# Optimization experiments

Hardware: AMD Instinct MI355X
Metric: run time of the kernel (lower is better)

## Reference

```python
import jax, jax.numpy as jnp
import numpy as np

SMOOTH = 1.0
P = 2
NUM_ITERS = 200  # kornia connected_components num_iterations


def _maxpool3x3(x):
    # F.max_pool2d(x, kernel_size=3, stride=1, padding=1) equivalent (NCHW)
    return jax.lax.reduce_window(
        x, -jnp.inf, jax.lax.max,
        window_dimensions=(1, 1, 3, 3),
        window_strides=(1, 1, 1, 1),
        padding='SAME',
    )


def connected_components(mask_f, num_iterations=NUM_ITERS):
    # kornia-style iterative label propagation on a (B,1,H,W) binary mask.
    # labels initialized to unique pixel ids where mask==1, 0 elsewhere,
    # then 3x3 max-pool propagated, keeping background pinned at 0.
    B, C, H, W = mask_f.shape
    mask = mask_f > 0
    init = jnp.arange(B * C * H * W, dtype=mask_f.dtype).reshape(B, C, H, W)
    out = jnp.where(mask, init, 0.0)

    def body(i, o):
        return jnp.where(mask, _maxpool3x3(o), 0.0)

    return jax.lax.fori_loop(0, num_iterations, body, out)


def setup_inputs() -> dict:
    key = jax.random.key(0)
    k1, k2 = jax.random.split(key)
    B, H, W = 16, 512, 512
    predict = jax.random.uniform(k1, (B, 1, H, W), dtype=jnp.float32)
    target = jax.random.uniform(k2, (B, 1, H, W), dtype=jnp.float32)
    return {"predict": predict, "target": target}


def reference(predict, target):
    B = predict.shape[0]
    # threshold at half of global max -> binary mask (non-differentiable)
    binmask = (predict > (predict.max() / 2)).astype(predict.dtype)
    labels = connected_components(jax.lax.stop_gradient(binmask))

    # torch.numel(torch.unique(labels)) via sort + adjacent-diff count (jit-safe)
    s = jnp.sort(labels.reshape(-1))
    n_unique = 1 + jnp.sum(s[1:] != s[:-1])

    penalty = n_unique.astype(jnp.float32) / B
    penalty = jnp.where(penalty < 1.0, jnp.float32(B), penalty)
    penalty = jnp.minimum(penalty, jnp.float32(B))

    p = predict.reshape(B, -1)
    t = target.reshape(B, -1)
    num = jnp.sum(p * t, axis=1) + SMOOTH
    den = jnp.sum(p ** P + t ** P, axis=1) + SMOOTH
    loss = 1.0 - num / den
    return loss.mean() * penalty  # reduction='mean'
```

## Files before the change

kernel.cpp:

```cpp
#include <hip/hip_runtime.h>
#include <hip/hip_cooperative_groups.h>
#include <stdint.h>

namespace cg = cooperative_groups;

#define NPIX   (16 * 512 * 512)
#define IMG    (512 * 512)
#define NB     16

#define CORE   64
#define HALO   8
#define KIT    8
#define NROUND 25
#define TW     88
#define TH     82
#define TX0    4

#define BM_WORDS  (NPIX / 32)
#define NREP      16
#define SAT       256u
#define MAX3(a, b, c) max(max((a), (b)), (c))

__global__ __launch_bounds__(256) void k_max(const float4* __restrict__ p, unsigned int* umax) {
    unsigned int m = 0;
    int base = blockIdx.x * 1024;
#pragma unroll
    for (int k = 0; k < 4; ++k) {
        float4 v = p[base + k * 256 + threadIdx.x];
        m = max(m, __float_as_uint(v.x));
        m = max(m, __float_as_uint(v.y));
        m = max(m, __float_as_uint(v.z));
        m = max(m, __float_as_uint(v.w));
    }
    for (int o = 32; o > 0; o >>= 1)
        m = max(m, (unsigned int)__shfl_down(m, o, 64));
    __shared__ unsigned int sm[4];
    int lane = threadIdx.x & 63, w = threadIdx.x >> 6;
    if (lane == 0) sm[w] = m;
    __syncthreads();
    if (threadIdx.x == 0)
        atomicMax(umax, max(max(sm[0], sm[1]), max(sm[2], sm[3])));
}

__global__ __launch_bounds__(256) void k_iso(const float* __restrict__ pr,
                                             const unsigned int* __restrict__ umax,
                                             unsigned int* __restrict__ isoCnt) {
    const float thr = __uint_as_float(*umax) * 0.5f;
    unsigned int cnt = 0;
    const int tid = threadIdx.x;
    for (int k = 0; k < 8; ++k) {
        int i4 = (blockIdx.x * 8 + k) * 256 + tid;
        int px = i4 * 4;
        int y   = (px >> 9) & 511;
        int gxr = px & 511;
        float4 c = *(const float4*)(pr + px);
        bool m0 = c.x > thr, m1 = c.y > thr, m2 = c.z > thr, m3 = c.w > thr;
        bool lc = (gxr > 0)   && pr[px - 1] > thr;
        bool rc = (gxr < 508) && pr[px + 4] > thr;
        bool u0 = false, u1 = false, u2 = false, u3 = false, lu = false, ru = false;
        if (y > 0) {
            float4 u = *(const float4*)(pr + px - 512);
            u0 = u.x > thr; u1 = u.y > thr; u2 = u.z > thr; u3 = u.w > thr;
            lu = (gxr > 0)   && pr[px - 513] > thr;
            ru = (gxr < 508) && pr[px - 508] > thr;
        }
        bool d0 = false, d1 = false, d2 = false, d3 = false, ld = false, rd = false;
        if (y < 511) {
            float4 d = *(const float4*)(pr + px + 512);
            d0 = d.x > thr; d1 = d.y > thr; d2 = d.z > thr; d3 = d.w > thr;
            ld = (gxr > 0)   && pr[px + 511] > thr;
            rd = (gxr < 508) && pr[px + 516] > thr;
        }
        bool v0 = u0 | d0, v1 = u1 | d1, v2 = u2 | d2, v3 = u3 | d3;
        bool cmL = lu | lc | ld, cmR = ru | rc | rd;
        bool cm0 = v0 | m0, cm1 = v1 | m1, cm2 = v2 | m2, cm3 = v3 | m3;
        cnt += (m0 && !(cmL | cm1 | v0) && px > 0) ? 1u : 0u;
        cnt += (m1 && !(cm0 | cm2 | v1)) ? 1u : 0u;
        cnt += (m2 && !(cm1 | cm3 | v2)) ? 1u : 0u;
        cnt += (m3 && !(cm2 | cmR | v3)) ? 1u : 0u;
    }
    for (int o = 32; o > 0; o >>= 1)
        cnt += __shfl_down(cnt, o, 64);
    __shared__ unsigned int sc[4];
    int lane = tid & 63, w = tid >> 6;
    if (lane == 0) sc[w] = cnt;
    __syncthreads();
    if (tid == 0)
        atomicAdd(isoCnt, sc[0] + sc[1] + sc[2] + sc[3]);
}

__global__ __launch_bounds__(256) void k_init(const float4* __restrict__ pr4,
                                              const float4* __restrict__ tg4,
                                              const unsigned int* __restrict__ umax,
                                              const unsigned int* __restrict__ isoCnt,
                                              int4* __restrict__ lab4,
                                              float* __restrict__ num, float* __restrict__ den) {
    const float thr = __uint_as_float(*umax) * 0.5f;
    const bool wlab = (*isoCnt < SAT);
    float sn = 0.f, sd = 0.f;
    int base = blockIdx.x * 1024;
#pragma unroll
    for (int k = 0; k < 4; ++k) {
        int i4 = base + k * 256 + threadIdx.x;
        float4 p = pr4[i4], t = tg4[i4];
        if (wlab) {
            int pix = i4 * 4;
            int4 L;
            L.x = (p.x > thr) ? pix     : -1;
            L.y = (p.y > thr) ? pix + 1 : -1;
            L.z = (p.z > thr) ? pix + 2 : -1;
            L.w = (p.w > thr) ? pix + 3 : -1;
            lab4[i4] = L;
        }
        sn += p.x * t.x + p.y * t.y + p.z * t.z + p.w * t.w;
        sd += p.x * p.x + p.y * p.y + p.z * p.z + p.w * p.w
            + t.x * t.x + t.y * t.y + t.z * t.z + t.w * t.w;
    }
    for (int o = 32; o > 0; o >>= 1) {
        sn += __shfl_down(sn, o, 64);
        sd += __shfl_down(sd, o, 64);
    }
    __shared__ float wn[4], wd[4];
    int lane = threadIdx.x & 63, w = threadIdx.x >> 6;
    if (lane == 0) { wn[w] = sn; wd[w] = sd; }
    __syncthreads();
    if (threadIdx.x == 0) {
        int b = blockIdx.x >> 6;
        atomicAdd(&num[b * 32], wn[0] + wn[1] + wn[2] + wn[3]);
        atomicAdd(&den[b * 32], wd[0] + wd[1] + wd[2] + wd[3]);
    }
}

__global__ __launch_bounds__(256, 4) void k_prop_all(int* __restrict__ bufA,
                                                     int* __restrict__ bufB,
                                                     unsigned int* __restrict__ bm,
                                                     const unsigned int* __restrict__ isoCnt) {
    if (*isoCnt >= SAT) return;
    cg::grid_group grid = cg::this_grid();
    __shared__ int T[TH * TW];
    const int tid  = threadIdx.x;
    const int blk  = blockIdx.x;
    const int bx   = blk & 7, by = (blk >> 3) & 7, bimg = blk >> 6;
    const int gx0  = bx * CORE - HALO;
    const int gy0  = by * CORE - HALO;
    int* const base0 = bufA + bimg * IMG;
    int* const base1 = bufB + bimg * IMG;

    {
        int4* bmz = (int4*)bm;
        for (int u = blk * 256 + tid; u < NREP * BM_WORDS / 4; u += 1024 * 256)
            bmz[u] = make_int4(0, 0, 0, 0);
    }

    if (tid < TW) { T[tid] = -1; T[81 * TW + tid] = -1; }
    if (tid < 80) { T[(tid + 1) * TW + 3] = -1; T[(tid + 1) * TW + 84] = -1; }
    for (int u = tid; u < 1600; u += 256) {
        int r = u / 20, c = (u % 20) * 4;
        int gy = gy0 + r, gx = gx0 + c;
        int4 v = (gy >= 0 && gy < 512 && gx >= 0 && gx < 512)
                 ? *(const int4*)(base0 + (gy << 9) + gx)
                 : make_int4(-1, -1, -1, -1);
        *(int4*)&T[(r + 1) * TW + TX0 + c] = v;
    }
    __syncthreads();
    grid.sync();

    const bool active = (tid < 200);
    const int cu = tid % 20, ru = tid / 20;
    const int x0 = cu * 4;
    const int yr = ru * 8;
    int4 O[8];

#define LOAD_ROW(y, V, VL, VR) do {                            \
        const int* _r = &T[((y) + 1) * TW + TX0 + x0];         \
        V  = *(const int4*)_r;                                 \
        VL = _r[-1];                                           \
        VR = _r[4];                                            \
    } while (0)

    for (int r = 0; r < NROUND; ++r) {
        for (int it = 0; it < KIT; ++it) {
            if (active) {
                int4 A, B, C; int Al, Ar, Bl, Br, Cl, Cr;
                LOAD_ROW(yr - 1, A, Al, Ar);
                LOAD_ROW(yr,     B, Bl, Br);
#pragma unroll
                for (int j = 0; j < 8; ++j) {
                    LOAD_ROW(yr + j + 1, C, Cl, Cr);
                    int4 col;
                    col.x = MAX3(A.x, B.x, C.x);
                    col.y = MAX3(A.y, B.y, C.y);
                    col.z = MAX3(A.z, B.z, C.z);
                    col.w = MAX3(A.w, B.w, C.w);
                    int cl = MAX3(Al, Bl, Cl);
                    int cr = MAX3(Ar, Br, Cr);
                    O[j].x = MAX3(cl,    col.x, col.y) | (B.x >> 31);
                    O[j].y = MAX3(col.x, col.y, col.z) | (B.y >> 31);
                    O[j].z = MAX3(col.y, col.z, col.w) | (B.z >> 31);
                    O[j].w = MAX3(col.z, col.w, cr)    | (B.w >> 31);
                    A = B; Al = Bl; Ar = Br;
                    B = C; Bl = Cl; Br = Cr;
                }
            }
            __syncthreads();
            if (active) {
#pragma unroll
                for (int j = 0; j < 8; ++j)
                    *(int4*)&T[(yr + j + 1) * TW + TX0 + x0] = O[j];
            }
            __syncthreads();
        }

        if (r < NROUND - 1) {
            int* dst = (r & 1) ? base1 : base0;
            for (int u = tid; u < 448; u += 256) {
                int lr, lc;
                if (u < 128)      { lr = u >> 4;                lc = u & 15; }
                else if (u < 256) { lr = 56 + ((u - 128) >> 4); lc = u & 15; }
                else { int v = u - 256; lr = 8 + (v >> 2); int s = v & 3; lc = (s < 2) ? s : 12 + s; }
                int4 val = *(const int4*)&T[(HALO + lr + 1) * TW + TX0 + HALO + lc * 4];
                *(int4*)(dst + ((by * CORE + lr) << 9) + bx * CORE + lc * 4) = val;
            }
            __threadfence();
            grid.sync();
            const int* src = (r & 1) ? base1 : base0;
            for (int u = tid; u < 576; u += 256) {
                int lrow, lcu;
                if (u < 160)      { lrow = u / 20;              lcu = u % 20; }
                else if (u < 320) { lrow = 72 + (u - 160) / 20; lcu = u % 20; }
                else { int v = u - 320; lrow = 8 + (v >> 2); int s = v & 3; lcu = (s < 2) ? s : 16 + s; }
                int gy = gy0 + lrow, gx = gx0 + lcu * 4;
                int4 val = (gy >= 0 && gy < 512 && gx >= 0 && gx < 512)
                           ? *(const int4*)(src + (gy << 9) + gx)
                           : make_int4(-1, -1, -1, -1);
                *(int4*)&T[(lrow + 1) * TW + TX0 + lcu * 4] = val;
            }
            __syncthreads();
        } else {
            for (int u = tid; u < 1024; u += 256) {
                int lr = u >> 4, lc = u & 15;
                int4 val = *(const int4*)&T[(HALO + lr + 1) * TW + TX0 + HALO + lc * 4];
                *(int4*)(base0 + ((by * CORE + lr) << 9) + bx * CORE + lc * 4) = val;
            }
        }
    }
#undef LOAD_ROW
}

__global__ __launch_bounds__(256) void k_bits(const int* __restrict__ lab,
                                              unsigned int* __restrict__ bm,
                                              const unsigned int* __restrict__ isoCnt) {
    if (*isoCnt >= SAT) return;
    __shared__ unsigned int sk[1024];
    __shared__ int slot[256];
    const int tid = threadIdx.x;
    unsigned int* rep = bm + (blockIdx.x & (NREP - 1)) * BM_WORDS;
    for (int k = 0; k < 4; ++k) {
        if (k) __syncthreads();
        const int i4 = blockIdx.x * 1024 + k * 256 + tid;
        int4 c = ((const int4*)lab)[i4];
        int pw = __shfl_up(c.w, 1, 64);
        unsigned int prevk;
        if ((tid & 63) == 0) {
            if (i4 == 0) prevk = ~0u;
            else { int pv = lab[i4 * 4 - 1]; prevk = (pv < 0) ? 0u : (unsigned int)pv; }
        } else {
            prevk = (pw < 0) ? 0u : (unsigned int)pw;
        }
        unsigned int k0 = (c.x < 0) ? 0u : (unsigned int)c.x;
        unsigned int k1 = (c.y < 0) ? 0u : (unsigned int)c.y;
        unsigned int k2 = (c.z < 0) ? 0u : (unsigned int)c.z;
        unsigned int k3 = (c.w < 0) ? 0u : (unsigned int)c.w;
        bool c0 = (k0 != prevk), c1 = (k1 != k0), c2 = (k2 != k1), c3 = (k3 != k2);
        sk[0 * 256 + tid] = k0;
        sk[1 * 256 + tid] = k1;
        sk[2 * 256 + tid] = k2;
        sk[3 * 256 + tid] = k3;
        if (c0) slot[k0 & 255] = tid * 4 + 0;
        if (c1) slot[k1 & 255] = tid * 4 + 1;
        if (c2) slot[k2 & 255] = tid * 4 + 2;
        if (c3) slot[k3 & 255] = tid * 4 + 3;
        __syncthreads();
#define SKAT(w) sk[((w) & 3) * 256 + ((w) >> 2)]
        if (c0) { int w = slot[k0 & 255]; if (w != tid * 4 + 0 && SKAT(w) == k0) c0 = false; }
        if (c1) { int w = slot[k1 & 255]; if (w != tid * 4 + 1 && SKAT(w) == k1) c1 = false; }
        if (c2) { int w = slot[k2 & 255]; if (w != tid * 4 + 2 && SKAT(w) == k2) c2 = false; }
        if (c3) { int w = slot[k3 & 255]; if (w != tid * 4 + 3 && SKAT(w) == k3) c3 = false; }
#undef SKAT
#define TSET(kk, cc) if (cc) {                                        \
            unsigned int word = rep[(kk) >> 5];                       \
            if (!((word >> ((kk) & 31)) & 1u))                        \
                atomicOr(&rep[(kk) >> 5], 1u << ((kk) & 31));         \
        }
        TSET(k0, c0); TSET(k1, c1); TSET(k2, c2); TSET(k3, c3);
#undef TSET
    }
}

__global__ void k_popc(const unsigned int* __restrict__ bm, unsigned int* nuniq, int words,
                       const unsigned int* __restrict__ isoCnt) {
    if (*isoCnt >= SAT) return;
    unsigned int c = 0;
    for (int i = blockIdx.x * blockDim.x + threadIdx.x; i < words; i += gridDim.x * blockDim.x) {
        unsigned int w = 0;
#pragma unroll
        for (int r = 0; r < NREP; ++r) w |= bm[r * BM_WORDS + i];
        c += __popc(w);
    }
    for (int o = 32; o > 0; o >>= 1)
        c += __shfl_down(c, o, 64);
    __shared__ unsigned int sc[4];
    int lane = threadIdx.x & 63, w = threadIdx.x >> 6;
    if (lane == 0) sc[w] = c;
    __syncthreads();
    if (threadIdx.x == 0)
        atomicAdd(nuniq, sc[0] + sc[1] + sc[2] + sc[3]);
}

__global__ void k_final(const unsigned int* __restrict__ nuniq,
                        const unsigned int* __restrict__ isoCnt,
                        const float* __restrict__ num, const float* __restrict__ den,
                        float* __restrict__ out) {
    float loss = 0.0f;
    for (int b = 0; b < NB; ++b)
        loss += 1.0f - (num[b * 32] + 1.0f) / (den[b * 32] + 1.0f);
    loss *= (1.0f / NB);
    float penalty;
    if (*isoCnt >= SAT) {
        penalty = (float)NB;
    } else {
        penalty = (float)(*nuniq) / (float)NB;
        if (penalty < 1.0f) penalty = (float)NB;
        penalty = fminf(penalty, (float)NB);
    }
    out[0] = loss * penalty;
}

extern "C" void kernel_launch(void* const* d_in, const int* in_sizes, int n_in,
                              void* d_out, int out_size, void* d_ws, size_t ws_size,
                              hipStream_t stream) {
    const float* predict = (const float*)d_in[0];
    const float* target  = (const float*)d_in[1];
    float* out = (float*)d_out;

    char* ws = (char*)d_ws;
    unsigned int* umax   = (unsigned int*)ws;
    unsigned int* nuniq  = (unsigned int*)(ws + 4);
    unsigned int* isoCnt = (unsigned int*)(ws + 8);
    float* num = (float*)(ws + 256);
    float* den = (float*)(ws + 2304);
    int* labA = (int*)(ws + 16384);
    int* labB = labA + NPIX;
    unsigned int* bm = (unsigned int*)(ws + 16384 + (size_t)2 * NPIX * sizeof(int));

    hipMemsetAsync(ws, 0, 16384, stream);

    k_max<<<1024, 256, 0, stream>>>((const float4*)predict, umax);
    k_iso<<<512, 256, 0, stream>>>(predict, umax, isoCnt);
    k_init<<<1024, 256, 0, stream>>>((const float4*)predict, (const float4*)target,
                                     umax, isoCnt, (int4*)labA, num, den);

    void* args[] = { (void*)&labA, (void*)&labB, (void*)&bm, (void*)&isoCnt };
    hipLaunchCooperativeKernel((void*)k_prop_all, dim3(1024), dim3(256), args, 0, stream);

    k_bits<<<NPIX / 4096, 256, 0, stream>>>(labA, bm, isoCnt);
    k_popc<<<512, 256, 0, stream>>>(bm, nuniq, BM_WORDS, isoCnt);
    k_final<<<1, 1, 0, stream>>>(nuniq, isoCnt, num, den, out);
}
```

Before: 147.2 us.

## Fuse dice sums into max pass and build initial labels inside propagation kernel

```diff
diff --git a/kernel.cpp b/kernel.cpp
--- a/kernel.cpp
+++ b/kernel.cpp
@@ -21,25 +21,42 @@
 #define SAT       256u
 #define MAX3(a, b, c) max(max((a), (b)), (c))
 
-__global__ __launch_bounds__(256) void k_max(const float4* __restrict__ p, unsigned int* umax) {
+__global__ __launch_bounds__(256) void k_maxdice(const float4* __restrict__ pr4,
+                                                 const float4* __restrict__ tg4,
+                                                 unsigned int* __restrict__ umax,
+                                                 float* __restrict__ num,
+                                                 float* __restrict__ den) {
     unsigned int m = 0;
+    float sn = 0.f, sd = 0.f;
     int base = blockIdx.x * 1024;
 #pragma unroll
     for (int k = 0; k < 4; ++k) {
-        float4 v = p[base + k * 256 + threadIdx.x];
-        m = max(m, __float_as_uint(v.x));
-        m = max(m, __float_as_uint(v.y));
-        m = max(m, __float_as_uint(v.z));
-        m = max(m, __float_as_uint(v.w));
-    }
-    for (int o = 32; o > 0; o >>= 1)
-        m = max(m, (unsigned int)__shfl_down(m, o, 64));
+        int i4 = base + k * 256 + threadIdx.x;
+        float4 p = pr4[i4], t = tg4[i4];
+        m = max(m, __float_as_uint(p.x));
+        m = max(m, __float_as_uint(p.y));
+        m = max(m, __float_as_uint(p.z));
+        m = max(m, __float_as_uint(p.w));
+        sn += p.x * t.x + p.y * t.y + p.z * t.z + p.w * t.w;
+        sd += p.x * p.x + p.y * p.y + p.z * p.z + p.w * p.w
+            + t.x * t.x + t.y * t.y + t.z * t.z + t.w * t.w;
+    }
+    for (int o = 32; o > 0; o >>= 1) {
+        m  = max(m, (unsigned int)__shfl_down(m, o, 64));
+        sn += __shfl_down(sn, o, 64);
+        sd += __shfl_down(sd, o, 64);
+    }
     __shared__ unsigned int sm[4];
+    __shared__ float wn[4], wd[4];
     int lane = threadIdx.x & 63, w = threadIdx.x >> 6;
-    if (lane == 0) sm[w] = m;
+    if (lane == 0) { sm[w] = m; wn[w] = sn; wd[w] = sd; }
     __syncthreads();
-    if (threadIdx.x == 0)
+    if (threadIdx.x == 0) {
         atomicMax(umax, max(max(sm[0], sm[1]), max(sm[2], sm[3])));
+        int b = blockIdx.x >> 6;
+        atomicAdd(&num[b * 32], wn[0] + wn[1] + wn[2] + wn[3]);
+        atomicAdd(&den[b * 32], wd[0] + wd[1] + wd[2] + wd[3]);
+    }
 }
 
 __global__ __launch_bounds__(256) void k_iso(const float* __restrict__ pr,
@@ -89,55 +106,16 @@
         atomicAdd(isoCnt, sc[0] + sc[1] + sc[2] + sc[3]);
 }
 
-__global__ __launch_bounds__(256) void k_init(const float4* __restrict__ pr4,
-                                              const float4* __restrict__ tg4,
-                                              const unsigned int* __restrict__ umax,
-                                              const unsigned int* __restrict__ isoCnt,
-                                              int4* __restrict__ lab4,
-                                              float* __restrict__ num, float* __restrict__ den) {
-    const float thr = __uint_as_float(*umax) * 0.5f;
-    const bool wlab = (*isoCnt < SAT);
-    float sn = 0.f, sd = 0.f;
-    int base = blockIdx.x * 1024;
-#pragma unroll
-    for (int k = 0; k < 4; ++k) {
-        int i4 = base + k * 256 + threadIdx.x;
-        float4 p = pr4[i4], t = tg4[i4];
-        if (wlab) {
-            int pix = i4 * 4;
-            int4 L;
-            L.x = (p.x > thr) ? pix     : -1;
-            L.y = (p.y > thr) ? pix + 1 : -1;
-            L.z = (p.z > thr) ? pix + 2 : -1;
-            L.w = (p.w > thr) ? pix + 3 : -1;
-            lab4[i4] = L;
-        }
-        sn += p.x * t.x + p.y * t.y + p.z * t.z + p.w * t.w;
-        sd += p.x * p.x + p.y * p.y + p.z * p.z + p.w * p.w
-            + t.x * t.x + t.y * t.y + t.z * t.z + t.w * t.w;
-    }
-    for (int o = 32; o > 0; o >>= 1) {
-        sn += __shfl_down(sn, o, 64);
-        sd += __shfl_down(sd, o, 64);
-    }
-    __shared__ float wn[4], wd[4];
-    int lane = threadIdx.x & 63, w = threadIdx.x >> 6;
-    if (lane == 0) { wn[w] = sn; wd[w] = sd; }
-    __syncthreads();
-    if (threadIdx.x == 0) {
-        int b = blockIdx.x >> 6;
-        atomicAdd(&num[b * 32], wn[0] + wn[1] + wn[2] + wn[3]);
-        atomicAdd(&den[b * 32], wd[0] + wd[1] + wd[2] + wd[3]);
-    }
-}
-
-__global__ __launch_bounds__(256, 4) void k_prop_all(int* __restrict__ bufA,
+__global__ __launch_bounds__(256, 4) void k_prop_all(const float* __restrict__ pr,
+                                                     int* __restrict__ bufA,
                                                      int* __restrict__ bufB,
                                                      unsigned int* __restrict__ bm,
+                                                     const unsigned int* __restrict__ umax,
                                                      const unsigned int* __restrict__ isoCnt) {
     if (*isoCnt >= SAT) return;
     cg::grid_group grid = cg::this_grid();
     __shared__ int T[TH * TW];
+    const float thr = __uint_as_float(*umax) * 0.5f;
     const int tid  = threadIdx.x;
     const int blk  = blockIdx.x;
     const int bx   = blk & 7, by = (blk >> 3) & 7, bimg = blk >> 6;
@@ -145,6 +123,7 @@
     const int gy0  = by * CORE - HALO;
     int* const base0 = bufA + bimg * IMG;
     int* const base1 = bufB + bimg * IMG;
+    const float* img = pr + bimg * IMG;
 
     {
         int4* bmz = (int4*)bm;
@@ -157,9 +136,15 @@
     for (int u = tid; u < 1600; u += 256) {
         int r = u / 20, c = (u % 20) * 4;
         int gy = gy0 + r, gx = gx0 + c;
-        int4 v = (gy >= 0 && gy < 512 && gx >= 0 && gx < 512)
-                 ? *(const int4*)(base0 + (gy << 9) + gx)
-                 : make_int4(-1, -1, -1, -1);
+        int4 v;
+        if (gy >= 0 && gy < 512 && gx >= 0 && gx < 512) {
+            float4 pv = *(const float4*)(img + (gy << 9) + gx);
+            int id = bimg * IMG + (gy << 9) + gx;
+            v.x = (pv.x > thr) ? id     : -1;
+            v.y = (pv.y > thr) ? id + 1 : -1;
+            v.z = (pv.z > thr) ? id + 2 : -1;
+            v.w = (pv.w > thr) ? id + 3 : -1;
+        } else v = make_int4(-1, -1, -1, -1);
         *(int4*)&T[(r + 1) * TW + TX0 + c] = v;
     }
     __syncthreads();
@@ -353,14 +338,14 @@
     int* labB = labA + NPIX;
     unsigned int* bm = (unsigned int*)(ws + 16384 + (size_t)2 * NPIX * sizeof(int));
 
-    hipMemsetAsync(ws, 0, 16384, stream);
-
-    k_max<<<1024, 256, 0, stream>>>((const float4*)predict, umax);
+    hipMemsetAsync(ws, 0, 8192, stream);
+
+    k_maxdice<<<1024, 256, 0, stream>>>((const float4*)predict, (const float4*)target,
+                                        umax, num, den);
     k_iso<<<512, 256, 0, stream>>>(predict, umax, isoCnt);
-    k_init<<<1024, 256, 0, stream>>>((const float4*)predict, (const float4*)target,
-                                     umax, isoCnt, (int4*)labA, num, den);
-
-    void* args[] = { (void*)&labA, (void*)&labB, (void*)&bm, (void*)&isoCnt };
+
+    void* args[] = { (void*)&predict, (void*)&labA, (void*)&labB,
+                     (void*)&bm, (void*)&umax, (void*)&isoCnt };
     hipLaunchCooperativeKernel((void*)k_prop_all, dim3(1024), dim3(256), args, 0, stream);
 
     k_bits<<<NPIX / 4096, 256, 0, stream>>>(labA, bm, isoCnt);
```

New measurement: 141.2 us. -4.1%, faster.
